# Optimization experiments

Measured on AMD Instinct MI355X. Metric: run time of the kernel, lower is better.

Reference implementation:

```python
import jax, jax.numpy as jnp
import numpy as np

DIM = 512
HEADS = 8
HEAD_DIM = 64
RS = 16        # region_size
EPEG_K = 15
L_TOKENS = 36864  # 192^2, multiple of RS^2 grid


def setup_inputs() -> dict:
    key = jax.random.key(0)
    ks = jax.random.split(key, 5)
    s = 1.0 / np.sqrt(DIM)
    x = jax.random.normal(ks[0], (1, L_TOKENS, DIM), jnp.float32)
    W_qkv = jax.random.normal(ks[1], (3 * HEADS * HEAD_DIM, DIM), jnp.float32) * s
    b_qkv = jnp.zeros((3 * HEADS * HEAD_DIM,), jnp.float32)
    W_proj = jax.random.normal(ks[2], (DIM, HEADS * HEAD_DIM), jnp.float32) * s
    b_proj = jnp.zeros((DIM,), jnp.float32)
    pe_w = jax.random.normal(ks[3], (HEADS, 1, EPEG_K, 1), jnp.float32) * 0.05
    pe_b = jnp.zeros((HEADS,), jnp.float32)
    return dict(x=x, W_qkv=W_qkv, b_qkv=b_qkv, W_proj=W_proj, b_proj=b_proj,
                pe_w=pe_w, pe_b=pe_b)


def reference(x, W_qkv, b_qkv, W_proj, b_proj, pe_w, pe_b):
    B, L, C = x.shape
    # --- padding() logic: square to HxW, H multiple of region_size ---
    H = int(np.ceil(np.sqrt(L)))
    H += (-H) % RS
    W = H
    add = H * W - L
    if add > 0:
        x = jnp.concatenate([x, jnp.zeros((B, add, C), x.dtype)], axis=1)
    # --- region_partition: (B,H,W,C) -> (num_regions*B, RS*RS, C) ---
    xr = (x.reshape(B, H // RS, RS, W // RS, RS, C)
            .transpose(0, 1, 3, 2, 4, 5)
            .reshape(-1, RS * RS, C))
    B_, N, _ = xr.shape
    # --- InnerAttention ---
    qkv = xr @ W_qkv.T + b_qkv                       # (B_, N, 3*h*d)
    qkv = qkv.reshape(B_, N, 3, HEADS, HEAD_DIM).transpose(2, 0, 3, 1, 4)
    q, k, v = qkv[0], qkv[1], qkv[2]                 # each (B_, h, N, d)
    scale = HEAD_DIM ** -0.5
    attn = jnp.einsum('bhid,bhjd->bhij', q * scale, k)   # (B_, h, N, N)
    # EPEG: depthwise conv (k,1) over the query axis of the score map
    pad = EPEG_K // 2
    pe = jax.lax.conv_general_dilated(
        attn, pe_w, window_strides=(1, 1), padding=((pad, pad), (0, 0)),
        dimension_numbers=('NCHW', 'OIHW', 'NCHW'), feature_group_count=HEADS)
    pe = pe + pe_b[None, :, None, None]
    attn = jax.nn.softmax(attn + pe, axis=-1)
    out = jnp.einsum('bhij,bhjd->bhid', attn, v)     # (B_, h, N, d)
    out = out.transpose(0, 2, 1, 3).reshape(B_, N, HEADS * HEAD_DIM)
    out = out @ W_proj.T + b_proj                    # (B_, N, C)
    # --- region_reverse ---
    out = (out.reshape(B, H // RS, W // RS, RS, RS, C)
              .transpose(0, 1, 3, 2, 4, 5)
              .reshape(B, H * W, C))
    if add > 0:
        out = out[:, :L]
    return out
```

## Files before the change

### kernel.cpp

```cpp
#include <hip/hip_runtime.h>
#include <stdint.h>

typedef __attribute__((ext_vector_type(8))) __bf16 bf16x8;
typedef __attribute__((ext_vector_type(16))) float f32x16;

__device__ __forceinline__ unsigned short f2bf(float f) {
  union { float f; unsigned int u; } v;
  v.f = f;
  unsigned int u = v.u;
  return (unsigned short)((u + 0x7FFFu + ((u >> 16) & 1u)) >> 16);
}

union BFrag { unsigned short u[8]; unsigned int w[4]; bf16x8 v; };

__device__ __forceinline__ f32x16 mfma32(bf16x8 a, bf16x8 b, f32x16 c) {
  return __builtin_amdgcn_mfma_f32_32x32x16_bf16(a, b, c, 0, 0, 0);
}

#define GLOAD_LDS16(gptr, lptr)                                                \
  __builtin_amdgcn_global_load_lds(                                           \
      (const __attribute__((address_space(1))) void*)(gptr),                  \
      (__attribute__((address_space(3))) void*)(lptr), 16, 0, 0)

__global__ __launch_bounds__(256) void k_xgather(const float* __restrict__ x,
                                                 unsigned short* __restrict__ xb) {
  int idx = blockIdx.x * 256 + threadIdx.x;
  int m = idx >> 6;
  int seg = (idx & 63) << 3;
  int r = m >> 8, n = m & 255;
  int a = r / 12, b = r - a * 12;
  int ii = n >> 4, jj = n & 15;
  long g = (long)((a * 16 + ii) * 192 + b * 16 + jj);
  const float4* p = (const float4*)(x + g * 512 + seg);
  float4 v0 = p[0], v1 = p[1];
  union { unsigned short u[8]; int4 v; } o;
  o.u[0] = f2bf(v0.x); o.u[1] = f2bf(v0.y); o.u[2] = f2bf(v0.z); o.u[3] = f2bf(v0.w);
  o.u[4] = f2bf(v1.x); o.u[5] = f2bf(v1.y); o.u[6] = f2bf(v1.z); o.u[7] = f2bf(v1.w);
  *(int4*)(xb + (size_t)m * 512 + seg) = o.v;
}

__global__ __launch_bounds__(256) void k_cvt(const float* __restrict__ s,
                                             unsigned short* __restrict__ d, int n8) {
  int i = blockIdx.x * 256 + threadIdx.x;
  if (i >= n8) return;
  const float4* p = (const float4*)(s + (size_t)i * 8);
  float4 a = p[0], b = p[1];
  union { unsigned short u[8]; int4 v; } o;
  o.u[0] = f2bf(a.x); o.u[1] = f2bf(a.y); o.u[2] = f2bf(a.z); o.u[3] = f2bf(a.w);
  o.u[4] = f2bf(b.x); o.u[5] = f2bf(b.y); o.u[6] = f2bf(b.z); o.u[7] = f2bf(b.w);
  *(int4*)(d + (size_t)i * 8) = o.v;
}

template<int MODE, int NBN>
__global__ __launch_bounds__(256, 2) void k_gemm(
    const unsigned short* __restrict__ A, const unsigned short* __restrict__ B,
    const float* __restrict__ bias,
    unsigned short* __restrict__ qb, unsigned short* __restrict__ kb,
    unsigned short* __restrict__ vtb, float* __restrict__ out) {
  __shared__ unsigned short As[8192];
  __shared__ unsigned short Bs[8192];
  int t = threadIdx.x;
  constexpr int NWG = NBN * 288;
  int d0 = blockIdx.x;
  int tl = (d0 & 7) * (NWG >> 3) + (d0 >> 3);
  int bm = tl / NBN, bn = tl % NBN;

  int w = t >> 6, lane = t & 63;
  int l31 = lane & 31, lh = lane >> 5;
  int wr = w >> 1, wc = w & 1;

  int srow = t >> 3, cseg = t & 7;
  int csw = (cseg ^ (srow & 7)) << 3;
  int ldsWaveOff = (t >> 6) << 10;

  f32x16 acc[2][2];
  for (int i = 0; i < 2; ++i)
    for (int j = 0; j < 2; ++j)
      for (int e = 0; e < 16; ++e) acc[i][j][e] = 0.0f;

  const unsigned short* Ag = A + (size_t)(bm * 128 + srow) * 512 + csw;
  const unsigned short* Bg = B + (size_t)(bn * 128 + srow) * 512 + csw;

  for (int ks = 0; ks < 8; ++ks) {
#pragma unroll
    for (int rnd = 0; rnd < 4; ++rnd) {
      GLOAD_LDS16(Ag + (size_t)rnd * 32 * 512 + ks * 64,
                  (char*)As + ldsWaveOff + rnd * 4096);
      GLOAD_LDS16(Bg + (size_t)rnd * 32 * 512 + ks * 64,
                  (char*)Bs + ldsWaveOff + rnd * 4096);
    }
    __syncthreads();
#pragma unroll
    for (int kt = 0; kt < 4; ++kt) {
      bf16x8 af[2], bfr[2];
#pragma unroll
      for (int mt = 0; mt < 2; ++mt) {
        int r = wr * 64 + mt * 32 + l31;
        af[mt] = *(const bf16x8*)((const char*)As + r * 128 +
                                  ((kt * 32 + lh * 16) ^ ((r & 7) << 4)));
      }
#pragma unroll
      for (int nt = 0; nt < 2; ++nt) {
        int r = wc * 64 + nt * 32 + l31;
        bfr[nt] = *(const bf16x8*)((const char*)Bs + r * 128 +
                                   ((kt * 32 + lh * 16) ^ ((r & 7) << 4)));
      }
#pragma unroll
      for (int mt = 0; mt < 2; ++mt)
#pragma unroll
        for (int nt = 0; nt < 2; ++nt)
          acc[mt][nt] = mfma32(af[mt], bfr[nt], acc[mt][nt]);
    }
    __syncthreads();
  }

  int nBase = bn * 128 + wc * 64;
  int mBase = bm * 128 + wr * 64;
#pragma unroll
  for (int nt = 0; nt < 2; ++nt) {
    int nn = nBase + nt * 32 + l31;
    float bs = bias[nn];
    if (MODE == 0) {
      int tsel = nn >> 9, rem = nn & 511;
      int hh = rem >> 6, d = rem & 63;
#pragma unroll
      for (int mt = 0; mt < 2; ++mt) {
#pragma unroll
        for (int q = 0; q < 4; ++q) {
          int m0 = mBase + mt * 32 + q * 8 + lh * 4;
          int r = m0 >> 8, tok = m0 & 255;
          size_t base = (size_t)(r * 8 + hh) * 16384;
          if (tsel == 0) {
#pragma unroll
            for (int j = 0; j < 4; ++j)
              qb[base + (size_t)(tok + j) * 64 + d] = f2bf((acc[mt][nt][q * 4 + j] + bs) * 0.125f);
          } else if (tsel == 1) {
#pragma unroll
            for (int j = 0; j < 4; ++j)
              kb[base + (size_t)(tok + j) * 64 + d] = f2bf(acc[mt][nt][q * 4 + j] + bs);
          } else {
            unsigned long long pv = 0;
#pragma unroll
            for (int j = 0; j < 4; ++j)
              pv |= (unsigned long long)f2bf(acc[mt][nt][q * 4 + j] + bs) << (16 * j);
            *(unsigned long long*)(vtb + base + (size_t)d * 256 + tok) = pv;
          }
        }
      }
    } else {
#pragma unroll
      for (int mt = 0; mt < 2; ++mt) {
#pragma unroll
        for (int q = 0; q < 4; ++q) {
          int m0 = mBase + mt * 32 + q * 8 + lh * 4;
          int r = m0 >> 8;
          int a = r / 12, bcol = r - a * 12;
#pragma unroll
          for (int j = 0; j < 4; ++j) {
            int tok = (m0 & 255) + j;
            int ii = tok >> 4, jj = tok & 15;
            long gg = (long)((a * 16 + ii) * 192 + bcol * 16 + jj);
            out[gg * 512 + nn] = acc[mt][nt][q * 4 + j] + bs;
          }
        }
      }
    }
  }
}

__global__ __launch_bounds__(512, 2) void k_attn5(
    const unsigned short* __restrict__ qb, const unsigned short* __restrict__ kb,
    const unsigned short* __restrict__ vtb, const float* __restrict__ pe_w,
    unsigned short* __restrict__ ctxb) {
  extern __shared__ char lds[];
  int rh = blockIdx.x;
  int h = rh & 7;
  int t = threadIdx.x, w = t >> 6, lane = t & 63;
  int l31 = lane & 31, lh = lane >> 5;
  int iw = w << 5;
  int myi = iw + l31;

  const unsigned short* Qg = qb + (size_t)rh * 16384;
  const unsigned short* Kg = kb + (size_t)rh * 16384;
  const unsigned short* Vg = vtb + (size_t)rh * 16384;
  const float* wh = pe_w + h * 15;

#pragma unroll
  for (int rr = 0; rr < 4; ++rr) {
    int row = rr * 64 + (t >> 3);
    GLOAD_LDS16(Kg + row * 64 + (((t & 7) ^ (row & 7)) << 3), lds + rr * 8192 + t * 16);
  }
  if (t < 96) {
    int dlo = t - 40, dhi = t - 39;
    unsigned int lo = (dlo >= 0 && dlo < 15) ? f2bf(wh[dlo]) : 0;
    unsigned int hi = (dhi >= 0 && dhi < 15) ? f2bf(wh[dhi]) : 0;
    *(unsigned int*)(lds + 73728 + t * 4) = lo | (hi << 16);
  }
  bf16x8 qf[4];
#pragma unroll
  for (int kt = 0; kt < 4; ++kt)
    qf[kt] = *(const bf16x8*)(Qg + (size_t)myi * 64 + kt * 16 + lh * 8);
  __syncthreads();

  float m = -3.0e38f, l = 0.0f;
  f32x16 acco[2];
#pragma unroll
  for (int nt = 0; nt < 2; ++nt)
#pragma unroll
    for (int e = 0; e < 16; ++e) acco[nt][e] = 0.0f;

#pragma unroll
  for (int tile = 0; tile < 4; ++tile) {
    f32x16 sacc[2];
#pragma unroll
    for (int jb = 0; jb < 2; ++jb)
#pragma unroll
      for (int e = 0; e < 16; ++e) sacc[jb][e] = 0.0f;
#pragma unroll
    for (int jb = 0; jb < 2; ++jb) {
      int kr = tile * 64 + jb * 32 + l31;
#pragma unroll
      for (int kt = 0; kt < 4; ++kt) {
        bf16x8 kf = *(const bf16x8*)(lds + kr * 128 + (((kt * 2 + lh) ^ (kr & 7)) << 4));
        sacc[jb] = mfma32(kf, qf[kt], sacc[jb]);
      }
    }
    __syncthreads();

    {
      int row = t >> 3;
      GLOAD_LDS16(Vg + row * 256 + tile * 64 + (((t & 7) ^ (row & 7)) << 3),
                  lds + 65536 + t * 16);
    }

    {
      int i2 = myi * 2;
#pragma unroll
      for (int jb = 0; jb < 2; ++jb)
#pragma unroll
        for (int rg = 0; rg < 16; ++rg) {
          int j = jb * 32 + (rg & 3) + 8 * (rg >> 2) + 4 * lh;
          *(unsigned short*)(lds + 32768 + j * 512 + (i2 ^ ((j & 7) << 4))) =
              f2bf(sacc[jb][rg]);
        }
    }
    __syncthreads();

#pragma unroll
    for (int jb = 0; jb < 2; ++jb) {
      int jr = jb * 32 + l31;
#pragma unroll
      for (int u = 0; u < 4; ++u) {
        int ktg = 2 * w + u - 1;
        if (ktg >= 0 && ktg < 16) {
          BFrag bb;
          int d0 = 16 * u + 8 * lh - l31 + 31;
#pragma unroll
          for (int e2 = 0; e2 < 4; ++e2)
            bb.w[e2] = *(const unsigned int*)(lds + 73728 + (d0 + 2 * e2) * 4);
          bf16x8 sfr = *(const bf16x8*)(lds + 32768 + jr * 512 +
                                        ((ktg * 32 + lh * 16) ^ ((jr & 7) << 4)));
          sacc[jb] = mfma32(sfr, bb.v, sacc[jb]);
        }
      }
    }

    unsigned int pk[2][8];
    {
      float pm = -3.0e38f;
#pragma unroll
      for (int jb = 0; jb < 2; ++jb)
#pragma unroll
        for (int e = 0; e < 16; ++e) pm = fmaxf(pm, sacc[jb][e]);
      pm = fmaxf(pm, __shfl_xor(pm, 32));
      float mn = fmaxf(m, pm);
      float f = __expf(m - mn);
      float ts = 0.0f;
#pragma unroll
      for (int jb = 0; jb < 2; ++jb)
#pragma unroll
        for (int u = 0; u < 8; ++u) {
          float p0 = __expf(sacc[jb][2 * u] - mn);
          float p1 = __expf(sacc[jb][2 * u + 1] - mn);
          ts += p0;
          ts += p1;
          pk[jb][u] = (unsigned int)f2bf(p0) | ((unsigned int)f2bf(p1) << 16);
        }
      ts += __shfl_xor(ts, 32);
      l = (tile == 0) ? ts : l * f + ts;
      m = mn;
      if (tile != 0) {
#pragma unroll
        for (int rg = 0; rg < 16; ++rg) {
          float g = __shfl(f, (rg & 3) + 8 * (rg >> 2) + 4 * lh);
          acco[0][rg] *= g;
          acco[1][rg] *= g;
        }
      }
    }

#pragma unroll
    for (int jb = 0; jb < 2; ++jb) {
      unsigned int sw[8];
#pragma unroll
      for (int u = 0; u < 8; ++u) sw[u] = (unsigned int)__shfl_xor((int)pk[jb][u], 32);
      BFrag pf0, pf1;
      if (lh == 0) {
        pf0.w[0] = pk[jb][0]; pf0.w[1] = pk[jb][1]; pf0.w[2] = sw[0]; pf0.w[3] = sw[1];
        pf1.w[0] = pk[jb][4]; pf1.w[1] = pk[jb][5]; pf1.w[2] = sw[4]; pf1.w[3] = sw[5];
      } else {
        pf0.w[0] = sw[2]; pf0.w[1] = sw[3]; pf0.w[2] = pk[jb][2]; pf0.w[3] = pk[jb][3];
        pf1.w[0] = sw[6]; pf1.w[1] = sw[7]; pf1.w[2] = pk[jb][6]; pf1.w[3] = pk[jb][7];
      }
#pragma unroll
      for (int nt = 0; nt < 2; ++nt) {
        int vr = nt * 32 + l31;
        int kj0 = jb * 2;
        bf16x8 vf0 = *(const bf16x8*)(lds + 65536 + vr * 128 +
                                      (((kj0 * 2 + lh) ^ (vr & 7)) << 4));
        bf16x8 vf1 = *(const bf16x8*)(lds + 65536 + vr * 128 +
                                      ((((kj0 + 1) * 2 + lh) ^ (vr & 7)) << 4));
        acco[nt] = mfma32(pf0.v, vf0, acco[nt]);
        acco[nt] = mfma32(pf1.v, vf1, acco[nt]);
      }
    }
  }

  float inv = 1.0f / l;
  int r256 = (rh >> 3) * 256;
  int chbase = h * 64;
#pragma unroll
  for (int rg = 0; rg < 16; ++rg) {
    int cr = (rg & 3) + 8 * (rg >> 2) + 4 * lh;
    float g = __shfl(inv, cr);
    int i = iw + cr;
    size_t rowoff = (size_t)(r256 + i) * 512 + chbase;
    ctxb[rowoff + l31] = f2bf(acco[0][rg] * g);
    ctxb[rowoff + 32 + l31] = f2bf(acco[1][rg] * g);
  }
}

extern "C" void kernel_launch(void* const* d_in, const int* in_sizes, int n_in,
                              void* d_out, int out_size, void* d_ws, size_t ws_size,
                              hipStream_t stream) {
  const float* x = (const float*)d_in[0];
  const float* Wqkv = (const float*)d_in[1];
  const float* bqkv = (const float*)d_in[2];
  const float* Wproj = (const float*)d_in[3];
  const float* bproj = (const float*)d_in[4];
  const float* pew = (const float*)d_in[5];

  char* ws = (char*)d_ws;
  unsigned short* xb = (unsigned short*)ws;
  unsigned short* wqkvb = (unsigned short*)(ws + 37748736);
  unsigned short* wprojb = (unsigned short*)(ws + 39321600);
  unsigned short* qb = (unsigned short*)(ws + 39845888);
  unsigned short* kb = (unsigned short*)(ws + 77594624);
  unsigned short* vtb = (unsigned short*)(ws + 115343360);

  (void)hipFuncSetAttribute((const void*)k_attn5,
                            hipFuncAttributeMaxDynamicSharedMemorySize, 163840);

  k_xgather<<<9216, 256, 0, stream>>>(x, xb);
  k_cvt<<<384, 256, 0, stream>>>(Wqkv, wqkvb, 98304);
  k_cvt<<<128, 256, 0, stream>>>(Wproj, wprojb, 32768);
  k_gemm<0, 12><<<3456, 256, 0, stream>>>(xb, wqkvb, bqkv, qb, kb, vtb, nullptr);
  k_attn5<<<1152, 512, 74112, stream>>>(qb, kb, vtb, pew, xb);
  k_gemm<1, 4><<<1152, 256, 0, stream>>>(xb, wprojb, bproj, nullptr, nullptr, nullptr,
                                         (float*)d_out);
}
```

Measured before the change: 221.6 us.

## Process attention key tiles in 32-column steps to shrink LDS and registers

The attention kernel now walks the 256 keys in eight 32-key steps instead of four 64-key steps. This halves the per-step score buffer and accumulator registers, and cuts dynamic LDS from about 74KB to about 58KB. Launch bounds go from 2 to 4 blocks per SM so more waves can be resident. In exchange there are twice as many online-softmax rescale steps and block-wide barriers per tile.

```diff
diff --git a/kernel.cpp b/kernel.cpp
--- a/kernel.cpp
+++ b/kernel.cpp
@@ -168,7 +168,7 @@
   }
 }
 
-__global__ __launch_bounds__(512, 2) void k_attn5(
+__global__ __launch_bounds__(512, 4) void k_attn6(
     const unsigned short* __restrict__ qb, const unsigned short* __restrict__ kb,
     const unsigned short* __restrict__ vtb, const float* __restrict__ pe_w,
     unsigned short* __restrict__ ctxb) {
@@ -194,7 +194,7 @@
     int dlo = t - 40, dhi = t - 39;
     unsigned int lo = (dlo >= 0 && dlo < 15) ? f2bf(wh[dlo]) : 0;
     unsigned int hi = (dhi >= 0 && dhi < 15) ? f2bf(wh[dhi]) : 0;
-    *(unsigned int*)(lds + 73728 + t * 4) = lo | (hi << 16);
+    *(unsigned int*)(lds + 57344 + t * 4) = lo | (hi << 16);
   }
   bf16x8 qf[4];
 #pragma unroll
@@ -210,45 +210,39 @@
     for (int e = 0; e < 16; ++e) acco[nt][e] = 0.0f;
 
 #pragma unroll
-  for (int tile = 0; tile < 4; ++tile) {
-    f32x16 sacc[2];
-#pragma unroll
-    for (int jb = 0; jb < 2; ++jb)
-#pragma unroll
-      for (int e = 0; e < 16; ++e) sacc[jb][e] = 0.0f;
-#pragma unroll
-    for (int jb = 0; jb < 2; ++jb) {
-      int kr = tile * 64 + jb * 32 + l31;
+  for (int it = 0; it < 8; ++it) {
+    f32x16 sacc;
+#pragma unroll
+    for (int e = 0; e < 16; ++e) sacc[e] = 0.0f;
+    {
+      int kr = it * 32 + l31;
 #pragma unroll
       for (int kt = 0; kt < 4; ++kt) {
         bf16x8 kf = *(const bf16x8*)(lds + kr * 128 + (((kt * 2 + lh) ^ (kr & 7)) << 4));
-        sacc[jb] = mfma32(kf, qf[kt], sacc[jb]);
+        sacc = mfma32(kf, qf[kt], sacc);
       }
     }
     __syncthreads();
 
-    {
+    if ((it & 1) == 0) {
       int row = t >> 3;
-      GLOAD_LDS16(Vg + row * 256 + tile * 64 + (((t & 7) ^ (row & 7)) << 3),
-                  lds + 65536 + t * 16);
+      GLOAD_LDS16(Vg + row * 256 + it * 32 + (((t & 7) ^ (row & 7)) << 3),
+                  lds + 49152 + t * 16);
     }
 
     {
       int i2 = myi * 2;
 #pragma unroll
-      for (int jb = 0; jb < 2; ++jb)
-#pragma unroll
-        for (int rg = 0; rg < 16; ++rg) {
-          int j = jb * 32 + (rg & 3) + 8 * (rg >> 2) + 4 * lh;
-          *(unsigned short*)(lds + 32768 + j * 512 + (i2 ^ ((j & 7) << 4))) =
-              f2bf(sacc[jb][rg]);
-        }
+      for (int rg = 0; rg < 16; ++rg) {
+        int jl = (rg & 3) + 8 * (rg >> 2) + 4 * lh;
+        *(unsigned short*)(lds + 32768 + jl * 512 + (i2 ^ ((jl & 7) << 4))) =
+            f2bf(sacc[rg]);
+      }
     }
     __syncthreads();
 
-#pragma unroll
-    for (int jb = 0; jb < 2; ++jb) {
-      int jr = jb * 32 + l31;
+    {
+      int jl = l31;
 #pragma unroll
       for (int u = 0; u < 4; ++u) {
         int ktg = 2 * w + u - 1;
@@ -257,39 +251,35 @@
           int d0 = 16 * u + 8 * lh - l31 + 31;
 #pragma unroll
           for (int e2 = 0; e2 < 4; ++e2)
-            bb.w[e2] = *(const unsigned int*)(lds + 73728 + (d0 + 2 * e2) * 4);
-          bf16x8 sfr = *(const bf16x8*)(lds + 32768 + jr * 512 +
-                                        ((ktg * 32 + lh * 16) ^ ((jr & 7) << 4)));
-          sacc[jb] = mfma32(sfr, bb.v, sacc[jb]);
+            bb.w[e2] = *(const unsigned int*)(lds + 57344 + (d0 + 2 * e2) * 4);
+          bf16x8 sfr = *(const bf16x8*)(lds + 32768 + jl * 512 +
+                                        ((ktg * 32 + lh * 16) ^ ((jl & 7) << 4)));
+          sacc = mfma32(sfr, bb.v, sacc);
         }
       }
     }
 
-    unsigned int pk[2][8];
+    unsigned int pk[8];
     {
       float pm = -3.0e38f;
 #pragma unroll
-      for (int jb = 0; jb < 2; ++jb)
-#pragma unroll
-        for (int e = 0; e < 16; ++e) pm = fmaxf(pm, sacc[jb][e]);
+      for (int e = 0; e < 16; ++e) pm = fmaxf(pm, sacc[e]);
       pm = fmaxf(pm, __shfl_xor(pm, 32));
       float mn = fmaxf(m, pm);
       float f = __expf(m - mn);
       float ts = 0.0f;
 #pragma unroll
-      for (int jb = 0; jb < 2; ++jb)
-#pragma unroll
-        for (int u = 0; u < 8; ++u) {
-          float p0 = __expf(sacc[jb][2 * u] - mn);
-          float p1 = __expf(sacc[jb][2 * u + 1] - mn);
-          ts += p0;
-          ts += p1;
-          pk[jb][u] = (unsigned int)f2bf(p0) | ((unsigned int)f2bf(p1) << 16);
-        }
+      for (int u = 0; u < 8; ++u) {
+        float p0 = __expf(sacc[2 * u] - mn);
+        float p1 = __expf(sacc[2 * u + 1] - mn);
+        ts += p0;
+        ts += p1;
+        pk[u] = (unsigned int)f2bf(p0) | ((unsigned int)f2bf(p1) << 16);
+      }
       ts += __shfl_xor(ts, 32);
-      l = (tile == 0) ? ts : l * f + ts;
+      l = (it == 0) ? ts : l * f + ts;
       m = mn;
-      if (tile != 0) {
+      if (it != 0) {
 #pragma unroll
         for (int rg = 0; rg < 16; ++rg) {
           float g = __shfl(f, (rg & 3) + 8 * (rg >> 2) + 4 * lh);
@@ -299,26 +289,25 @@
       }
     }
 
-#pragma unroll
-    for (int jb = 0; jb < 2; ++jb) {
+    {
       unsigned int sw[8];
 #pragma unroll
-      for (int u = 0; u < 8; ++u) sw[u] = (unsigned int)__shfl_xor((int)pk[jb][u], 32);
+      for (int u = 0; u < 8; ++u) sw[u] = (unsigned int)__shfl_xor((int)pk[u], 32);
       BFrag pf0, pf1;
       if (lh == 0) {
-        pf0.w[0] = pk[jb][0]; pf0.w[1] = pk[jb][1]; pf0.w[2] = sw[0]; pf0.w[3] = sw[1];
-        pf1.w[0] = pk[jb][4]; pf1.w[1] = pk[jb][5]; pf1.w[2] = sw[4]; pf1.w[3] = sw[5];
+        pf0.w[0] = pk[0]; pf0.w[1] = pk[1]; pf0.w[2] = sw[0]; pf0.w[3] = sw[1];
+        pf1.w[0] = pk[4]; pf1.w[1] = pk[5]; pf1.w[2] = sw[4]; pf1.w[3] = sw[5];
       } else {
-        pf0.w[0] = sw[2]; pf0.w[1] = sw[3]; pf0.w[2] = pk[jb][2]; pf0.w[3] = pk[jb][3];
-        pf1.w[0] = sw[6]; pf1.w[1] = sw[7]; pf1.w[2] = pk[jb][6]; pf1.w[3] = pk[jb][7];
-      }
+        pf0.w[0] = sw[2]; pf0.w[1] = sw[3]; pf0.w[2] = pk[2]; pf0.w[3] = pk[3];
+        pf1.w[0] = sw[6]; pf1.w[1] = sw[7]; pf1.w[2] = pk[6]; pf1.w[3] = pk[7];
+      }
+      int kj0 = (it & 1) * 2;
 #pragma unroll
       for (int nt = 0; nt < 2; ++nt) {
         int vr = nt * 32 + l31;
-        int kj0 = jb * 2;
-        bf16x8 vf0 = *(const bf16x8*)(lds + 65536 + vr * 128 +
+        bf16x8 vf0 = *(const bf16x8*)(lds + 49152 + vr * 128 +
                                       (((kj0 * 2 + lh) ^ (vr & 7)) << 4));
-        bf16x8 vf1 = *(const bf16x8*)(lds + 65536 + vr * 128 +
+        bf16x8 vf1 = *(const bf16x8*)(lds + 49152 + vr * 128 +
                                       ((((kj0 + 1) * 2 + lh) ^ (vr & 7)) << 4));
         acco[nt] = mfma32(pf0.v, vf0, acco[nt]);
         acco[nt] = mfma32(pf1.v, vf1, acco[nt]);
@@ -358,14 +347,14 @@
   unsigned short* kb = (unsigned short*)(ws + 77594624);
   unsigned short* vtb = (unsigned short*)(ws + 115343360);
 
-  (void)hipFuncSetAttribute((const void*)k_attn5,
+  (void)hipFuncSetAttribute((const void*)k_attn6,
                             hipFuncAttributeMaxDynamicSharedMemorySize, 163840);
 
   k_xgather<<<9216, 256, 0, stream>>>(x, xb);
   k_cvt<<<384, 256, 0, stream>>>(Wqkv, wqkvb, 98304);
   k_cvt<<<128, 256, 0, stream>>>(Wproj, wprojb, 32768);
   k_gemm<0, 12><<<3456, 256, 0, stream>>>(xb, wqkvb, bqkv, qb, kb, vtb, nullptr);
-  k_attn5<<<1152, 512, 74112, stream>>>(qb, kb, vtb, pew, xb);
+  k_attn6<<<1152, 512, 57728, stream>>>(qb, kb, vtb, pew, xb);
   k_gemm<1, 4><<<1152, 256, 0, stream>>>(xb, wprojb, bproj, nullptr, nullptr, nullptr,
                                          (float*)d_out);
 }
```

Measured after the change: 244.7 us. +10.4%, slower.
